# Kernel tuning notes

Hardware: AMD Instinct MI355X
Metric: run time of the kernel (lower is better)

## Reference

```python
import jax, jax.numpy as jnp
import numpy as np
import math

NUM_HEADS = 8


def _dwconv(x, w, b, pad):
    # depthwise conv: x (B,C,H,W), w (C,1,k,k)
    c = x.shape[1]
    y = jax.lax.conv_general_dilated(
        x, w, window_strides=(1, 1), padding=[(pad, pad), (pad, pad)],
        feature_group_count=c, dimension_numbers=("NCHW", "OIHW", "NCHW"))
    return y + b[None, :, None, None]


def _conv(x, w, b, pad):
    y = jax.lax.conv_general_dilated(
        x, w, window_strides=(1, 1), padding=[(pad, pad), (pad, pad)],
        dimension_numbers=("NCHW", "OIHW", "NCHW"))
    return y + b[None, :, None, None]


def setup_inputs() -> dict:
    key = jax.random.key(0)
    ks = jax.random.split(key, 6)
    B, C, H, W = 8, 128, 128, 128
    x = jax.random.normal(ks[0], (B, C, H, W), dtype=jnp.float32)
    wq = jax.random.normal(ks[1], (C, 1, 9, 9), dtype=jnp.float32) * 0.05
    wk = jax.random.normal(ks[2], (C, 1, 9, 9), dtype=jnp.float32) * 0.05
    wv = jax.random.normal(ks[3], (C, 1, 9, 9), dtype=jnp.float32) * 0.05
    wo = jax.random.normal(ks[4], (C, C, 3, 3), dtype=jnp.float32) * 0.02
    bq = jnp.zeros((C,), jnp.float32)
    bk = jnp.zeros((C,), jnp.float32)
    bv = jnp.zeros((C,), jnp.float32)
    bo = jnp.zeros((C,), jnp.float32)
    return {"x": x, "wq": wq, "bq": bq, "wk": wk, "bk": bk,
            "wv": wv, "bv": bv, "wo": wo, "bo": bo}


def reference(x, wq, bq, wk, bk, wv, bv, wo, bo):
    b, c, h, w = x.shape
    hds = NUM_HEADS
    d = (h * w) // hds  # spatial dim split across heads
    q = _dwconv(x, wq, bq, 4).reshape(b, c, hds, d).transpose(0, 2, 1, 3)  # (b,hds,c,d)
    k = _dwconv(x, wk, bk, 4).reshape(b, c, hds, d).transpose(0, 2, 3, 1)  # (b,hds,d,c)
    v = _dwconv(x, wv, bv, 4).reshape(b, c, hds, d).transpose(0, 2, 1, 3)  # (b,hds,c,d)
    # channel attention: C x C scores per head, fp32 softmax
    qk = jnp.einsum("bhcd,bhde->bhce", q.astype(jnp.float32), k.astype(jnp.float32)) / math.sqrt(h * w)
    a = jnp.einsum("bhce,bhed->bhcd", jax.nn.softmax(qk, axis=-1), v.astype(jnp.float32))
    a = a.transpose(0, 2, 1, 3).reshape(b, c, h, w)
    return _conv(a, wo, bo, 1)
```

## Files before the change

kernel.cpp:

```cpp
#include <hip/hip_runtime.h>

#define BATCH 8
#define CH 128
#define HH 128
#define WW 128
#define HWSZ 16384
#define NHEADS 8
#define DHEAD 2048

typedef short bf16x8 __attribute__((ext_vector_type(8)));
typedef short bf16x4v __attribute__((ext_vector_type(4)));
typedef float f32x4 __attribute__((ext_vector_type(4)));
typedef float f32x2 __attribute__((ext_vector_type(2)));
typedef _Float16 f16x8 __attribute__((ext_vector_type(8)));
typedef _Float16 f16x4 __attribute__((ext_vector_type(4)));

static __device__ inline unsigned short f2bf(float f) {
    unsigned u = __builtin_bit_cast(unsigned, f);
    u += 0x7fff + ((u >> 16) & 1);
    return (unsigned short)(u >> 16);
}

__global__ __launch_bounds__(256) void toeplitz_prep_kernel(
    const float* __restrict__ wq, const float* __restrict__ wk,
    const float* __restrict__ wv, _Float16* __restrict__ Tp)
{
    const int g = blockIdx.x * 256 + threadIdx.x;
    const int c    = g / 1728;
    const int rem  = g - c * 1728;
    const int m    = rem >> 6;
    const int lane = rem & 63;
    const int conv = m / 9;
    const int dy   = m - conv * 9;
    const float* w = (conv == 0) ? wq : ((conv == 1) ? wk : wv);
    const int j    = lane & 15;
    const int kb   = (lane >> 4) << 3;
    f16x8 h;
    #pragma unroll
    for (int e = 0; e < 8; ++e) {
        const int d = kb + e - j;
        h[e] = (d >= 0 && d <= 8) ? (_Float16)w[c * 81 + dy * 9 + d]
                                  : (_Float16)0.f;
    }
    *(f16x8*)&Tp[(size_t)g * 8] = h;
}

__global__ __launch_bounds__(256) void dwconv_qkv_mfma_kernel(
    const float* __restrict__ x,
    const float* __restrict__ bq, const float* __restrict__ bk,
    const float* __restrict__ bv,
    const _Float16* __restrict__ Tp,
    unsigned short* __restrict__ Qb, unsigned short* __restrict__ Kb,
    unsigned short* __restrict__ Vb)
{
    const int bc = blockIdx.x;
    const int b  = bc >> 7;
    const int c  = bc & (CH - 1);

    __shared__ _Float16 img[136][144];

    const int tid  = threadIdx.x;
    const int wave = tid >> 6;
    const int lane = tid & 63;
    const int lx   = lane & 15;
    const int qd   = lane >> 4;

    f16x8 Btp[27];
    const _Float16* tp = Tp + (size_t)c * 13824 + (size_t)lane * 8;
    #pragma unroll
    for (int m = 0; m < 27; ++m)
        Btp[m] = *(const f16x8*)(tp + (size_t)m * 512);

    {
        f16x8 z = {0, 0, 0, 0, 0, 0, 0, 0};
        _Float16* flat = &img[0][0];
        for (int i = tid; i < 2448; i += 256)
            *(f16x8*)&flat[i * 8] = z;
    }
    __syncthreads();
    const float* xp = x + (size_t)bc * HWSZ;
    for (int i = tid; i < 4096; i += 256) {
        const float4 v = *(const float4*)&xp[i * 4];
        const int y  = i >> 5;
        const int xc = (i & 31) << 2;
        f16x4 h = {(_Float16)v.x, (_Float16)v.y, (_Float16)v.z, (_Float16)v.w};
        *(f16x4*)&img[y + 4][xc + 4] = h;
    }
    __syncthreads();

    const float bqv = bq[c], bkv = bk[c], bvv = bv[c];

    #pragma unroll 1
    for (int t = 0; t < 8; ++t) {
        const int sg = t * 4 + wave;
        const int yg = sg >> 2;
        const int y0 = yg << 4;
        const int x0 = (sg & 3) << 5;

        f32x4 aq0 = {bqv, bqv, bqv, bqv}, aq1 = aq0;
        f32x4 ak0 = {bkv, bkv, bkv, bkv}, ak1 = ak0;
        f32x4 av0 = {bvv, bvv, bvv, bvv}, av1 = av0;

        const _Float16* rp = &img[y0 + lx][x0 + (qd << 3)];
        #pragma unroll
        for (int dy = 0; dy < 9; ++dy) {
            const f16x8 a0 = *(const f16x8*)rp;
            const f16x8 a1 = *(const f16x8*)(rp + 16);
            rp += 144;
            aq0 = __builtin_amdgcn_mfma_f32_16x16x32_f16(a0, Btp[dy],      aq0, 0, 0, 0);
            aq1 = __builtin_amdgcn_mfma_f32_16x16x32_f16(a1, Btp[dy],      aq1, 0, 0, 0);
            ak0 = __builtin_amdgcn_mfma_f32_16x16x32_f16(a0, Btp[9 + dy],  ak0, 0, 0, 0);
            ak1 = __builtin_amdgcn_mfma_f32_16x16x32_f16(a1, Btp[9 + dy],  ak1, 0, 0, 0);
            av0 = __builtin_amdgcn_mfma_f32_16x16x32_f16(a0, Btp[18 + dy], av0, 0, 0, 0);
            av1 = __builtin_amdgcn_mfma_f32_16x16x32_f16(a1, Btp[18 + dy], av1, 0, 0, 0);
        }

        const size_t base = ((size_t)(b * 8 + yg) * CH + c) * DHEAD
                          + (size_t)(qd << 2) * WW + x0 + lx;
        #pragma unroll
        for (int r = 0; r < 4; ++r) {
            Qb[base + r * WW]      = f2bf(aq0[r]);
            Qb[base + r * WW + 16] = f2bf(aq1[r]);
            Kb[base + r * WW]      = f2bf(ak0[r]);
            Kb[base + r * WW + 16] = f2bf(ak1[r]);
            Vb[base + r * WW]      = f2bf(av0[r]);
            Vb[base + r * WW + 16] = f2bf(av1[r]);
        }
    }
}

__global__ __launch_bounds__(256) void qks_kernel(
    const unsigned short* __restrict__ Qb, const unsigned short* __restrict__ Kb,
    unsigned short* __restrict__ Pb)
{
    const int o    = blockIdx.x;
    const int bh   = o & 63;
    const int c0   = (o >> 6) << 4;

    __shared__ __align__(16) char smem[36864];

    const int tid  = threadIdx.x;
    const int wave = tid >> 6;
    const int lane = tid & 63;
    const int lx   = lane & 15;
    const int qd   = lane >> 4;
    const int n0   = wave << 5;

    f32x4 acc0 = {0.f, 0.f, 0.f, 0.f}, acc1 = acc0;

    const unsigned short* Qp = Qb + ((size_t)bh * CH + c0) * DHEAD;
    const unsigned short* Kp = Kb + (size_t)bh * CH * DHEAD;

    const int qr = tid >> 4, qu = tid & 15;
    const unsigned qoff = (unsigned)((qr << 8) + (qu << 4)) ^ (((unsigned)qr & 7u) << 4);

    #pragma unroll 1
    for (int chk = 0; chk < 16; ++chk) {
        const int t0 = chk << 7;
        __syncthreads();
        {
            const bf16x8 v = *(const bf16x8*)&Qp[(size_t)qr * DHEAD + t0 + qu * 8];
            *(bf16x8*)(smem + qoff) = v;
        }
        for (int i = tid; i < 2048; i += 256) {
            const int r = i >> 4, u = i & 15;
            const bf16x8 v = *(const bf16x8*)&Kp[(size_t)r * DHEAD + t0 + u * 8];
            const unsigned off = 4096u +
                ((unsigned)((r << 8) + (u << 4)) ^ (((unsigned)r & 7u) << 4));
            *(bf16x8*)(smem + off) = v;
        }
        __syncthreads();
        #pragma unroll
        for (int ki = 0; ki < 4; ++ki) {
            const int kcb = (ki * 32 + qd * 8) << 1;
            const bf16x8 a = *(const bf16x8*)(smem +
                ((unsigned)((lx << 8) + kcb) ^ (((unsigned)lx & 7u) << 4)));
            const int r0 = n0 + lx, r1 = n0 + 16 + lx;
            const bf16x8 b0 = *(const bf16x8*)(smem + 4096u +
                ((unsigned)((r0 << 8) + kcb) ^ (((unsigned)r0 & 7u) << 4)));
            const bf16x8 b1 = *(const bf16x8*)(smem + 4096u +
                ((unsigned)((r1 << 8) + kcb) ^ (((unsigned)r1 & 7u) << 4)));
            acc0 = __builtin_amdgcn_mfma_f32_16x16x32_bf16(a, b0, acc0, 0, 0, 0);
            acc1 = __builtin_amdgcn_mfma_f32_16x16x32_bf16(a, b1, acc1, 0, 0, 0);
        }
    }

    __syncthreads();
    float* Ss = (float*)smem;
    #pragma unroll
    for (int r = 0; r < 4; ++r) {
        Ss[(qd * 4 + r) * 132 + n0 + lx]      = acc0[r];
        Ss[(qd * 4 + r) * 132 + n0 + 16 + lx] = acc1[r];
    }
    __syncthreads();

    const int rr = tid >> 4;
    const int c8 = (tid & 15) << 3;
    f32x4 v0 = *(const f32x4*)&Ss[rr * 132 + c8];
    f32x4 v1 = *(const f32x4*)&Ss[rr * 132 + c8 + 4];
    const f32x4 sc = {0.0078125f, 0.0078125f, 0.0078125f, 0.0078125f};
    v0 *= sc; v1 *= sc;
    float m = fmaxf(fmaxf(fmaxf(v0[0], v0[1]), fmaxf(v0[2], v0[3])),
                    fmaxf(fmaxf(v1[0], v1[1]), fmaxf(v1[2], v1[3])));
    m = fmaxf(m, __shfl_xor(m, 1));
    m = fmaxf(m, __shfl_xor(m, 2));
    m = fmaxf(m, __shfl_xor(m, 4));
    m = fmaxf(m, __shfl_xor(m, 8));
    float e[8];
    #pragma unroll
    for (int j = 0; j < 4; ++j) {
        e[j]     = __expf(v0[j] - m);
        e[4 + j] = __expf(v1[j] - m);
    }
    float s = 0.f;
    #pragma unroll
    for (int j = 0; j < 8; ++j) s += e[j];
    s += __shfl_xor(s, 1);
    s += __shfl_xor(s, 2);
    s += __shfl_xor(s, 4);
    s += __shfl_xor(s, 8);
    const float inv = 1.f / s;
    bf16x8 h;
    #pragma unroll
    for (int j = 0; j < 8; ++j) h[j] = (short)f2bf(e[j] * inv);
    *(bf16x8*)&Pb[((size_t)bh * CH + c0 + rr) * CH + c8] = h;
}

__global__ __launch_bounds__(256) void pv_mfma_kernel(
    const unsigned short* __restrict__ Pb, const unsigned short* __restrict__ Vb,
    unsigned short* __restrict__ At)
{
    const int blk = blockIdx.x;
    const int t0  = (blk & 15) << 7;
    const int bh  = blk >> 4;

    __shared__ __align__(16) char smem[69632];
    unsigned short (*Ps)[136] = (unsigned short(*)[136])smem;
    unsigned short (*Vs)[136] = (unsigned short(*)[136])(smem + 34816);
    float (*So)[132] = (float(*)[132])smem;

    const int tid  = threadIdx.x;
    const int wave = tid >> 6;
    const int lane = tid & 63;
    const int lx   = lane & 15;
    const int qd   = lane >> 4;
    const int m0   = (wave & 1) * 64;
    const int n0   = (wave >> 1) * 64;

    const unsigned short* Pp = Pb + (size_t)bh * CH * CH;
    const unsigned short* Vp = Vb + (size_t)bh * CH * DHEAD;

    for (int i = tid; i < 2048; i += 256) {
        const int r  = i >> 4;
        const int cl = (i & 15) << 3;
        *(bf16x8*)&Ps[r][cl] = *(const bf16x8*)&Pp[(size_t)r * CH + cl];
    }
    for (int i = tid; i < 2048; i += 256) {
        const int e   = i & 127;
        const int tc8 = (i >> 7) << 3;
        const bf16x8 vv = *(const bf16x8*)&Vp[(size_t)e * DHEAD + t0 + tc8];
        #pragma unroll
        for (int j = 0; j < 8; ++j) Vs[tc8 + j][e] = (unsigned short)vv[j];
    }
    __syncthreads();

    f32x4 acc[4][4];
    #pragma unroll
    for (int mi = 0; mi < 4; ++mi)
        #pragma unroll
        for (int ni = 0; ni < 4; ++ni) acc[mi][ni] = (f32x4){0.f, 0.f, 0.f, 0.f};

    #pragma unroll
    for (int ki = 0; ki < 4; ++ki) {
        const int kc = ki * 32 + qd * 8;
        bf16x8 a[4], bv[4];
        #pragma unroll
        for (int mi = 0; mi < 4; ++mi)
            a[mi] = *(const bf16x8*)&Ps[m0 + mi * 16 + lx][kc];
        #pragma unroll
        for (int ni = 0; ni < 4; ++ni)
            bv[ni] = *(const bf16x8*)&Vs[n0 + ni * 16 + lx][kc];
        #pragma unroll
        for (int mi = 0; mi < 4; ++mi)
            #pragma unroll
            for (int ni = 0; ni < 4; ++ni)
                acc[mi][ni] = __builtin_amdgcn_mfma_f32_16x16x32_bf16(
                    a[mi], bv[ni], acc[mi][ni], 0, 0, 0);
    }

    __syncthreads();
    #pragma unroll
    for (int mi = 0; mi < 4; ++mi)
        #pragma unroll
        for (int ni = 0; ni < 4; ++ni)
            #pragma unroll
            for (int r = 0; r < 4; ++r)
                So[n0 + ni * 16 + lx][m0 + mi * 16 + qd * 4 + r] = acc[mi][ni][r];
    __syncthreads();

    const int t  = tid >> 1;
    const int ch = (tid & 1) * 64;
    const size_t orow = (((size_t)(bh >> 3) * HWSZ) + (size_t)(bh & 7) * DHEAD + t0 + t) * CH + ch;
    #pragma unroll
    for (int j = 0; j < 8; ++j) {
        const float4 f0 = *(const float4*)&So[t][ch + j * 8];
        const float4 f1 = *(const float4*)&So[t][ch + j * 8 + 4];
        bf16x8 h;
        h[0] = (short)f2bf(f0.x); h[1] = (short)f2bf(f0.y);
        h[2] = (short)f2bf(f0.z); h[3] = (short)f2bf(f0.w);
        h[4] = (short)f2bf(f1.x); h[5] = (short)f2bf(f1.y);
        h[6] = (short)f2bf(f1.z); h[7] = (short)f2bf(f1.w);
        *(bf16x8*)&At[orow + j * 8] = h;
    }
}

__global__ __launch_bounds__(256) void wprep_kernel(
    const float* __restrict__ wo, unsigned short* __restrict__ Wt)
{
    const int i = blockIdx.x * 256 + threadIdx.x;
    const int tap = i >> 14;
    const int rem = i & 16383;
    const int co  = rem >> 7;
    const int ci  = rem & 127;
    Wt[i] = f2bf(wo[(size_t)(co * CH + ci) * 9 + tap]);
}

__global__ __launch_bounds__(512, 2) void conv3x3_mfma_kernel(
    const unsigned short* __restrict__ At, const unsigned short* __restrict__ Wt,
    const float* __restrict__ bo, float* __restrict__ out)
{
    __shared__ __align__(16) char smem[163840];

    const int w    = ((blockIdx.x & 7) << 6) | (blockIdx.x >> 3);
    const int yp   = w & 63;
    const int b    = w >> 6;
    const int y0   = yp << 1;

    const int tid  = threadIdx.x;
    const int wave = tid >> 6;
    const int lane = tid & 63;
    const int lx   = lane & 15;
    const int qd   = lane >> 4;
    const int m0   = (wave & 1) << 6;
    const int n0   = (wave >> 1) << 6;
    const int rsel = n0 >> 7;
    const int xb   = n0 & 64;

    const int j0 = tid, j1 = tid + 512;
    const int co0 = j0 >> 3, cu0 = j0 & 7;
    const int co1 = j1 >> 3, cu1 = j1 & 7;
    const unsigned swo0 = (unsigned)((co0 * 128 + cu0 * 16) ^ ((co0 & 7) << 4)) + 131072u;
    const unsigned swo1 = (unsigned)((co1 * 128 + cu1 * 16) ^ ((co1 & 7) << 4)) + 131072u;

    float4 nwa = *(const float4*)&Wt[(size_t)co0 * 128 + cu0 * 8];
    float4 nwb = *(const float4*)&Wt[(size_t)co1 * 128 + cu1 * 8];

    const size_t abase = (size_t)b * HWSZ * CH;
    for (int i = tid; i < 8192; i += 512) {
        const int r   = i >> 11;
        const int rem = i & 2047;
        const int xx  = rem >> 4;
        const int u   = rem & 15;
        const int gy  = y0 - 1 + r;
        float4 v = make_float4(0.f, 0.f, 0.f, 0.f);
        if ((unsigned)gy < HH)
            v = *(const float4*)&At[abase + (size_t)gy * WW * CH + xx * CH + u * 8];
        const int xp = xx + 1;
        const unsigned off = (unsigned)((r << 15) + (xx << 8) + (u << 4))
                           ^ (((unsigned)xp & 7u) << 4);
        *(float4*)(smem + off) = v;
    }
    *(float4*)(smem + swo0) = nwa;
    *(float4*)(smem + swo1) = nwb;
    nwa = *(const float4*)&Wt[(size_t)co0 * 128 + 64 + cu0 * 8];
    nwb = *(const float4*)&Wt[(size_t)co1 * 128 + 64 + cu1 * 8];

    f32x4 acc[4][4];
    #pragma unroll
    for (int mi = 0; mi < 4; ++mi) {
        f32x4 bv;
        #pragma unroll
        for (int r = 0; r < 4; ++r) bv[r] = bo[m0 + mi * 16 + qd * 4 + r];
        #pragma unroll
        for (int ni = 0; ni < 4; ++ni) acc[mi][ni] = bv;
    }

    __syncthreads();

    #pragma unroll 1
    for (int s = 0; s < 18; ++s) {
        const int tap = s >> 1;
        const int dy  = (tap * 11) >> 5;
        const int txc = tap - dy * 3;
        const int kh  = s & 1;
        const int ra  = rsel + dy;
        const unsigned wbase = 131072u + (unsigned)(s & 1) * 16384u;

        #pragma unroll
        for (int ks = 0; ks < 2; ++ks) {
            const int wkb = ks * 64 + qd * 16;
            const int akb = kh * 128 + ks * 64 + qd * 16;
            bf16x8 a[4], bfr[4];
            #pragma unroll
            for (int mi = 0; mi < 4; ++mi) {
                const int co = m0 + mi * 16 + lx;
                a[mi] = *(const bf16x8*)(smem + wbase +
                        (unsigned)((co * 128 + wkb) ^ ((co & 7) << 4)));
            }
            #pragma unroll
            for (int ni = 0; ni < 4; ++ni) {
                const int xp = xb + ni * 16 + lx + txc;
                const bool z = (unsigned)(xp - 1) >= 128u;
                const int xpc = z ? 1 : xp;
                const unsigned off = (unsigned)((ra << 15) + ((xpc - 1) << 8) + akb)
                                   ^ (((unsigned)xpc & 7u) << 4);
                bfr[ni] = *(const bf16x8*)(smem + off);
                if (z) bfr[ni] = (bf16x8){0, 0, 0, 0, 0, 0, 0, 0};
            }
            #pragma unroll
            for (int mi = 0; mi < 4; ++mi)
                #pragma unroll
                for (int ni = 0; ni < 4; ++ni)
                    acc[mi][ni] = __builtin_amdgcn_mfma_f32_16x16x32_bf16(
                        a[mi], bfr[ni], acc[mi][ni], 0, 0, 0);
        }
        if (s < 17) {
            const unsigned nb = 131072u + (unsigned)((s + 1) & 1) * 16384u;
            *(float4*)(smem + (swo0 - 131072u) + nb) = nwa;
            *(float4*)(smem + (swo1 - 131072u) + nb) = nwb;
            if (s < 16) {
                const int s2 = s + 2;
                const size_t gb = (size_t)(s2 >> 1) * 16384 + (s2 & 1) * 64;
                nwa = *(const float4*)&Wt[gb + co0 * 128 + cu0 * 8];
                nwb = *(const float4*)&Wt[gb + co1 * 128 + cu1 * 8];
            }
        }
        __syncthreads();
    }

    const int gy = y0 + rsel;
    const size_t obase = (size_t)b * CH * HWSZ + (size_t)gy * WW + xb;
    #pragma unroll
    for (int mi = 0; mi < 4; ++mi) {
        #pragma unroll
        for (int r = 0; r < 4; ++r) {
            const int co = m0 + mi * 16 + qd * 4 + r;
            float* orow = out + obase + (size_t)co * HWSZ;
            #pragma unroll
            for (int ni = 0; ni < 4; ++ni)
                orow[ni * 16 + lx] = acc[mi][ni][r];
        }
    }
}

extern "C" void kernel_launch(void* const* d_in, const int* in_sizes, int n_in,
                              void* d_out, int out_size, void* d_ws, size_t ws_size,
                              hipStream_t stream)
{
    const float* x  = (const float*)d_in[0];
    const float* wq = (const float*)d_in[1];
    const float* bq = (const float*)d_in[2];
    const float* wk = (const float*)d_in[3];
    const float* bk = (const float*)d_in[4];
    const float* wv = (const float*)d_in[5];
    const float* bv = (const float*)d_in[6];
    const float* wo = (const float*)d_in[7];
    const float* bo = (const float*)d_in[8];

    char* ws = (char*)d_ws;
    unsigned short* Qb    = (unsigned short*)(ws);
    unsigned short* Kb    = (unsigned short*)(ws + (size_t)33554432);
    unsigned short* Vb    = (unsigned short*)(ws + (size_t)67108864);
    unsigned short* Pb    = (unsigned short*)(ws + (size_t)134217728);
    unsigned short* At    = (unsigned short*)(ws + (size_t)136314880);
    unsigned short* Wt    = (unsigned short*)(ws + (size_t)169869312);
    _Float16*       Tp    = (_Float16*)      (ws + (size_t)100663296);

    toeplitz_prep_kernel<<<864, 256, 0, stream>>>(wq, wk, wv, Tp);
    dwconv_qkv_mfma_kernel<<<BATCH * CH, 256, 0, stream>>>(x, bq, bk, bv, Tp, Qb, Kb, Vb);
    wprep_kernel<<<576, 256, 0, stream>>>(wo, Wt);
    qks_kernel<<<512, 256, 0, stream>>>(Qb, Kb, Pb);
    pv_mfma_kernel<<<64 * 16, 256, 0, stream>>>(Pb, Vb, At);
    conv3x3_mfma_kernel<<<BATCH * 64, 512, 0, stream>>>(At, Wt, bo, (float*)d_out);
}
```

Before: 277.6 us.

## Read conv3x3 activations directly from global memory and raise occupancy targets

The 3x3 output conv no longer stages a 4-row activation halo in LDS. Each wave now loads its B fragments straight from global memory, with bounds masking, which cuts LDS use from 160KB to 32KB so more blocks can be resident. The launch-bound occupancy hints are raised on both the conv3x3 kernel (4 blocks) and the depthwise QKV kernel (2 blocks). The QKV epilogue also switches to the packed v_cvt_pk_bf16_f32 conversion. The trade-off is that the MFMA loop now sees global-memory latency without explicit prefetch, and the tighter register budget from the higher occupancy hint may force the 64-float accumulator to spill.

```diff
diff --git a/kernel.cpp b/kernel.cpp
--- a/kernel.cpp
+++ b/kernel.cpp
@@ -19,6 +19,12 @@
     unsigned u = __builtin_bit_cast(unsigned, f);
     u += 0x7fff + ((u >> 16) & 1);
     return (unsigned short)(u >> 16);
+}
+
+static __device__ inline unsigned cvtpk(float lo, float hi) {
+    unsigned r;
+    asm("v_cvt_pk_bf16_f32 %0, %1, %2" : "=v"(r) : "v"(lo), "v"(hi));
+    return r;
 }
 
 __global__ __launch_bounds__(256) void toeplitz_prep_kernel(
@@ -45,7 +51,7 @@
     *(f16x8*)&Tp[(size_t)g * 8] = h;
 }
 
-__global__ __launch_bounds__(256) void dwconv_qkv_mfma_kernel(
+__global__ __launch_bounds__(256, 2) void dwconv_qkv_mfma_kernel(
     const float* __restrict__ x,
     const float* __restrict__ bq, const float* __restrict__ bk,
     const float* __restrict__ bv,
@@ -118,13 +124,25 @@
         const size_t base = ((size_t)(b * 8 + yg) * CH + c) * DHEAD
                           + (size_t)(qd << 2) * WW + x0 + lx;
         #pragma unroll
-        for (int r = 0; r < 4; ++r) {
-            Qb[base + r * WW]      = f2bf(aq0[r]);
-            Qb[base + r * WW + 16] = f2bf(aq1[r]);
-            Kb[base + r * WW]      = f2bf(ak0[r]);
-            Kb[base + r * WW + 16] = f2bf(ak1[r]);
-            Vb[base + r * WW]      = f2bf(av0[r]);
-            Vb[base + r * WW + 16] = f2bf(av1[r]);
+        for (int rp2 = 0; rp2 < 4; rp2 += 2) {
+            const unsigned pq0 = cvtpk(aq0[rp2], aq0[rp2 + 1]);
+            const unsigned pq1 = cvtpk(aq1[rp2], aq1[rp2 + 1]);
+            const unsigned pk0 = cvtpk(ak0[rp2], ak0[rp2 + 1]);
+            const unsigned pk1 = cvtpk(ak1[rp2], ak1[rp2 + 1]);
+            const unsigned pv0 = cvtpk(av0[rp2], av0[rp2 + 1]);
+            const unsigned pv1 = cvtpk(av1[rp2], av1[rp2 + 1]);
+            Qb[base + rp2 * WW]            = (unsigned short)pq0;
+            Qb[base + (rp2 + 1) * WW]      = (unsigned short)(pq0 >> 16);
+            Qb[base + rp2 * WW + 16]       = (unsigned short)pq1;
+            Qb[base + (rp2 + 1) * WW + 16] = (unsigned short)(pq1 >> 16);
+            Kb[base + rp2 * WW]            = (unsigned short)pk0;
+            Kb[base + (rp2 + 1) * WW]      = (unsigned short)(pk0 >> 16);
+            Kb[base + rp2 * WW + 16]       = (unsigned short)pk1;
+            Kb[base + (rp2 + 1) * WW + 16] = (unsigned short)(pk1 >> 16);
+            Vb[base + rp2 * WW]            = (unsigned short)pv0;
+            Vb[base + (rp2 + 1) * WW]      = (unsigned short)(pv0 >> 16);
+            Vb[base + rp2 * WW + 16]       = (unsigned short)pv1;
+            Vb[base + (rp2 + 1) * WW + 16] = (unsigned short)(pv1 >> 16);
         }
     }
 }
@@ -325,11 +343,11 @@
     Wt[i] = f2bf(wo[(size_t)(co * CH + ci) * 9 + tap]);
 }
 
-__global__ __launch_bounds__(512, 2) void conv3x3_mfma_kernel(
+__global__ __launch_bounds__(512, 4) void conv3x3_mfma_kernel(
     const unsigned short* __restrict__ At, const unsigned short* __restrict__ Wt,
     const float* __restrict__ bo, float* __restrict__ out)
 {
-    __shared__ __align__(16) char smem[163840];
+    __shared__ __align__(16) char smem[32768];
 
     const int w    = ((blockIdx.x & 7) << 6) | (blockIdx.x >> 3);
     const int yp   = w & 63;
@@ -349,27 +367,11 @@
     const int j0 = tid, j1 = tid + 512;
     const int co0 = j0 >> 3, cu0 = j0 & 7;
     const int co1 = j1 >> 3, cu1 = j1 & 7;
-    const unsigned swo0 = (unsigned)((co0 * 128 + cu0 * 16) ^ ((co0 & 7) << 4)) + 131072u;
-    const unsigned swo1 = (unsigned)((co1 * 128 + cu1 * 16) ^ ((co1 & 7) << 4)) + 131072u;
+    const unsigned swo0 = (unsigned)((co0 * 128 + cu0 * 16) ^ ((co0 & 7) << 4));
+    const unsigned swo1 = (unsigned)((co1 * 128 + cu1 * 16) ^ ((co1 & 7) << 4));
 
     float4 nwa = *(const float4*)&Wt[(size_t)co0 * 128 + cu0 * 8];
     float4 nwb = *(const float4*)&Wt[(size_t)co1 * 128 + cu1 * 8];
-
-    const size_t abase = (size_t)b * HWSZ * CH;
-    for (int i = tid; i < 8192; i += 512) {
-        const int r   = i >> 11;
-        const int rem = i & 2047;
-        const int xx  = rem >> 4;
-        const int u   = rem & 15;
-        const int gy  = y0 - 1 + r;
-        float4 v = make_float4(0.f, 0.f, 0.f, 0.f);
-        if ((unsigned)gy < HH)
-            v = *(const float4*)&At[abase + (size_t)gy * WW * CH + xx * CH + u * 8];
-        const int xp = xx + 1;
-        const unsigned off = (unsigned)((r << 15) + (xx << 8) + (u << 4))
-                           ^ (((unsigned)xp & 7u) << 4);
-        *(float4*)(smem + off) = v;
-    }
     *(float4*)(smem + swo0) = nwa;
     *(float4*)(smem + swo1) = nwb;
     nwa = *(const float4*)&Wt[(size_t)co0 * 128 + 64 + cu0 * 8];
@@ -384,6 +386,8 @@
         #pragma unroll
         for (int ni = 0; ni < 4; ++ni) acc[mi][ni] = bv;
     }
+
+    const unsigned short* Ab = At + (size_t)b * HWSZ * CH;
 
     __syncthreads();
 
@@ -393,13 +397,15 @@
         const int dy  = (tap * 11) >> 5;
         const int txc = tap - dy * 3;
         const int kh  = s & 1;
-        const int ra  = rsel + dy;
-        const unsigned wbase = 131072u + (unsigned)(s & 1) * 16384u;
+        const int gy  = y0 - 1 + rsel + dy;
+        const bool rok = (unsigned)gy < HH;
+        const unsigned short* Arow = Ab + (size_t)gy * (WW * CH);
+        const unsigned wbase = (unsigned)(s & 1) * 16384u;
+        const int cis = kh * 64 + qd * 8;
 
         #pragma unroll
         for (int ks = 0; ks < 2; ++ks) {
             const int wkb = ks * 64 + qd * 16;
-            const int akb = kh * 128 + ks * 64 + qd * 16;
             bf16x8 a[4], bfr[4];
             #pragma unroll
             for (int mi = 0; mi < 4; ++mi) {
@@ -409,13 +415,10 @@
             }
             #pragma unroll
             for (int ni = 0; ni < 4; ++ni) {
-                const int xp = xb + ni * 16 + lx + txc;
-                const bool z = (unsigned)(xp - 1) >= 128u;
-                const int xpc = z ? 1 : xp;
-                const unsigned off = (unsigned)((ra << 15) + ((xpc - 1) << 8) + akb)
-                                   ^ (((unsigned)xpc & 7u) << 4);
-                bfr[ni] = *(const bf16x8*)(smem + off);
-                if (z) bfr[ni] = (bf16x8){0, 0, 0, 0, 0, 0, 0, 0};
+                const int xx = xb + ni * 16 + lx + txc - 1;
+                bfr[ni] = (bf16x8){0, 0, 0, 0, 0, 0, 0, 0};
+                if (rok && (unsigned)xx < WW)
+                    bfr[ni] = *(const bf16x8*)&Arow[(size_t)xx * CH + cis + ks * 32];
             }
             #pragma unroll
             for (int mi = 0; mi < 4; ++mi)
@@ -425,9 +428,9 @@
                         a[mi], bfr[ni], acc[mi][ni], 0, 0, 0);
         }
         if (s < 17) {
-            const unsigned nb = 131072u + (unsigned)((s + 1) & 1) * 16384u;
-            *(float4*)(smem + (swo0 - 131072u) + nb) = nwa;
-            *(float4*)(smem + (swo1 - 131072u) + nb) = nwb;
+            const unsigned nb = (unsigned)((s + 1) & 1) * 16384u;
+            *(float4*)(smem + nb + swo0) = nwa;
+            *(float4*)(smem + nb + swo1) = nwb;
             if (s < 16) {
                 const int s2 = s + 2;
                 const size_t gb = (size_t)(s2 >> 1) * 16384 + (s2 & 1) * 64;
```

Result: slower. 309.6 us (+11.5%).

## Stage Toeplitz weights in LDS and pad conv tile to drop boundary checks

Applied to the files above, without the earlier changes.

The depthwise QKV kernel stops keeping 27 f16x8 Toeplitz fragments in registers. It copies them to shared memory and reloads three per tap, which lowers register pressure and may raise occupancy but adds LDS traffic and a larger LDS footprint. The 3x3 conv kernel now stores explicit zero-padded halo columns in shared memory, removing per-fragment bounds checks and zero selects. In exchange it drops the double-buffered weight slice for a single buffer with two barriers per step, which serialises weight staging with compute.

```diff
diff --git a/kernel.cpp b/kernel.cpp
--- a/kernel.cpp
+++ b/kernel.cpp
@@ -58,6 +58,7 @@
     const int c  = bc & (CH - 1);
 
     __shared__ _Float16 img[136][144];
+    __shared__ _Float16 tps[13824];
 
     const int tid  = threadIdx.x;
     const int wave = tid >> 6;
@@ -65,12 +66,11 @@
     const int lx   = lane & 15;
     const int qd   = lane >> 4;
 
-    f16x8 Btp[27];
-    const _Float16* tp = Tp + (size_t)c * 13824 + (size_t)lane * 8;
-    #pragma unroll
-    for (int m = 0; m < 27; ++m)
-        Btp[m] = *(const f16x8*)(tp + (size_t)m * 512);
-
+    {
+        const _Float16* tg = Tp + (size_t)c * 13824;
+        for (int i = tid; i < 1728; i += 256)
+            *(f16x8*)&tps[i * 8] = *(const f16x8*)&tg[i * 8];
+    }
     {
         f16x8 z = {0, 0, 0, 0, 0, 0, 0, 0};
         _Float16* flat = &img[0][0];
@@ -89,6 +89,7 @@
     __syncthreads();
 
     const float bqv = bq[c], bkv = bk[c], bvv = bv[c];
+    const _Float16* tl = tps + lane * 8;
 
     #pragma unroll 1
     for (int t = 0; t < 8; ++t) {
@@ -107,12 +108,15 @@
             const f16x8 a0 = *(const f16x8*)rp;
             const f16x8 a1 = *(const f16x8*)(rp + 16);
             rp += 144;
-            aq0 = __builtin_amdgcn_mfma_f32_16x16x32_f16(a0, Btp[dy],      aq0, 0, 0, 0);
-            aq1 = __builtin_amdgcn_mfma_f32_16x16x32_f16(a1, Btp[dy],      aq1, 0, 0, 0);
-            ak0 = __builtin_amdgcn_mfma_f32_16x16x32_f16(a0, Btp[9 + dy],  ak0, 0, 0, 0);
-            ak1 = __builtin_amdgcn_mfma_f32_16x16x32_f16(a1, Btp[9 + dy],  ak1, 0, 0, 0);
-            av0 = __builtin_amdgcn_mfma_f32_16x16x32_f16(a0, Btp[18 + dy], av0, 0, 0, 0);
-            av1 = __builtin_amdgcn_mfma_f32_16x16x32_f16(a1, Btp[18 + dy], av1, 0, 0, 0);
+            const f16x8 bq_ = *(const f16x8*)(tl + dy * 512);
+            const f16x8 bk_ = *(const f16x8*)(tl + (9 + dy) * 512);
+            const f16x8 bv_ = *(const f16x8*)(tl + (18 + dy) * 512);
+            aq0 = __builtin_amdgcn_mfma_f32_16x16x32_f16(a0, bq_, aq0, 0, 0, 0);
+            aq1 = __builtin_amdgcn_mfma_f32_16x16x32_f16(a1, bq_, aq1, 0, 0, 0);
+            ak0 = __builtin_amdgcn_mfma_f32_16x16x32_f16(a0, bk_, ak0, 0, 0, 0);
+            ak1 = __builtin_amdgcn_mfma_f32_16x16x32_f16(a1, bk_, ak1, 0, 0, 0);
+            av0 = __builtin_amdgcn_mfma_f32_16x16x32_f16(a0, bv_, av0, 0, 0, 0);
+            av1 = __builtin_amdgcn_mfma_f32_16x16x32_f16(a1, bv_, av1, 0, 0, 0);
         }
 
         const size_t base = ((size_t)(b * 8 + yg) * CH + c) * DHEAD
@@ -329,7 +333,7 @@
     const unsigned short* __restrict__ At, const unsigned short* __restrict__ Wt,
     const float* __restrict__ bo, float* __restrict__ out)
 {
-    __shared__ __align__(16) char smem[163840];
+    __shared__ __align__(16) char smem[149504];
 
     const int w    = ((blockIdx.x & 7) << 6) | (blockIdx.x >> 3);
     const int yp   = w & 63;
@@ -349,13 +353,21 @@
     const int j0 = tid, j1 = tid + 512;
     const int co0 = j0 >> 3, cu0 = j0 & 7;
     const int co1 = j1 >> 3, cu1 = j1 & 7;
-    const unsigned swo0 = (unsigned)((co0 * 128 + cu0 * 16) ^ ((co0 & 7) << 4)) + 131072u;
-    const unsigned swo1 = (unsigned)((co1 * 128 + cu1 * 16) ^ ((co1 & 7) << 4)) + 131072u;
+    const unsigned swo0 = (unsigned)((co0 * 128 + cu0 * 16) ^ ((co0 & 7) << 4)) + 133120u;
+    const unsigned swo1 = (unsigned)((co1 * 128 + cu1 * 16) ^ ((co1 & 7) << 4)) + 133120u;
 
     float4 nwa = *(const float4*)&Wt[(size_t)co0 * 128 + cu0 * 8];
     float4 nwb = *(const float4*)&Wt[(size_t)co1 * 128 + cu1 * 8];
 
     const size_t abase = (size_t)b * HWSZ * CH;
+    if (tid < 128) {
+        const int r  = tid >> 5;
+        const int cu = tid & 31;
+        const int xp = (cu & 16) ? 129 : 0;
+        const int u  = cu & 15;
+        const unsigned off = (unsigned)(r * 33280 + xp * 256 + u * 16) ^ (((unsigned)xp & 7u) << 4);
+        *(float4*)(smem + off) = make_float4(0.f, 0.f, 0.f, 0.f);
+    }
     for (int i = tid; i < 8192; i += 512) {
         const int r   = i >> 11;
         const int rem = i & 2047;
@@ -366,8 +378,7 @@
         if ((unsigned)gy < HH)
             v = *(const float4*)&At[abase + (size_t)gy * WW * CH + xx * CH + u * 8];
         const int xp = xx + 1;
-        const unsigned off = (unsigned)((r << 15) + (xx << 8) + (u << 4))
-                           ^ (((unsigned)xp & 7u) << 4);
+        const unsigned off = (unsigned)(r * 33280 + xp * 256 + u * 16) ^ (((unsigned)xp & 7u) << 4);
         *(float4*)(smem + off) = v;
     }
     *(float4*)(smem + swo0) = nwa;
@@ -394,7 +405,6 @@
         const int txc = tap - dy * 3;
         const int kh  = s & 1;
         const int ra  = rsel + dy;
-        const unsigned wbase = 131072u + (unsigned)(s & 1) * 16384u;
 
         #pragma unroll
         for (int ks = 0; ks < 2; ++ks) {
@@ -404,18 +414,15 @@
             #pragma unroll
             for (int mi = 0; mi < 4; ++mi) {
                 const int co = m0 + mi * 16 + lx;
-                a[mi] = *(const bf16x8*)(smem + wbase +
+                a[mi] = *(const bf16x8*)(smem + 133120u +
                         (unsigned)((co * 128 + wkb) ^ ((co & 7) << 4)));
             }
             #pragma unroll
             for (int ni = 0; ni < 4; ++ni) {
                 const int xp = xb + ni * 16 + lx + txc;
-                const bool z = (unsigned)(xp - 1) >= 128u;
-                const int xpc = z ? 1 : xp;
-                const unsigned off = (unsigned)((ra << 15) + ((xpc - 1) << 8) + akb)
-                                   ^ (((unsigned)xpc & 7u) << 4);
+                const unsigned off = (unsigned)(ra * 33280 + xp * 256 + akb)
+                                   ^ (((unsigned)xp & 7u) << 4);
                 bfr[ni] = *(const bf16x8*)(smem + off);
-                if (z) bfr[ni] = (bf16x8){0, 0, 0, 0, 0, 0, 0, 0};
             }
             #pragma unroll
             for (int mi = 0; mi < 4; ++mi)
@@ -424,18 +431,18 @@
                     acc[mi][ni] = __builtin_amdgcn_mfma_f32_16x16x32_bf16(
                         a[mi], bfr[ni], acc[mi][ni], 0, 0, 0);
         }
+        __syncthreads();
         if (s < 17) {
-            const unsigned nb = 131072u + (unsigned)((s + 1) & 1) * 16384u;
-            *(float4*)(smem + (swo0 - 131072u) + nb) = nwa;
-            *(float4*)(smem + (swo1 - 131072u) + nb) = nwb;
+            *(float4*)(smem + swo0) = nwa;
+            *(float4*)(smem + swo1) = nwb;
             if (s < 16) {
                 const int s2 = s + 2;
                 const size_t gb = (size_t)(s2 >> 1) * 16384 + (s2 & 1) * 64;
                 nwa = *(const float4*)&Wt[gb + co0 * 128 + cu0 * 8];
                 nwb = *(const float4*)&Wt[gb + co1 * 128 + cu1 * 8];
             }
-        }
-        __syncthreads();
+            __syncthreads();
+        }
     }
 
     const int gy = y0 + rsel;
```

New measurement: 278.3 us. Within noise of the previous version (+0.2%).
